# Performance work log

Hardware: AMD Instinct MI355X
Metric: run time of the kernel (lower is better)

## Reference

```python
import jax, jax.numpy as jnp
import numpy as np

B = 131072
D = 256
N_SC = 16
SC_CAP = 2
MAX_USERS = 8
POW_DIM = 10


def setup_inputs() -> dict:
    key = jax.random.key(0)
    k0, k1, k2, k3 = jax.random.split(key, 4)
    x = jax.random.normal(k0, (B, D), dtype=jnp.float32)
    available_actions = jax.random.randint(k1, (B, 2 * MAX_USERS), 0, 2).astype(jnp.int32)
    # per-head Categorical weights: Linear(D, action_dim), small init (gain=0.01 orthogonal-ish)
    W_sc = jax.random.normal(k2, (MAX_USERS, D, N_SC), dtype=jnp.float32) * 0.01
    b_sc = jnp.zeros((MAX_USERS, N_SC), dtype=jnp.float32)
    W_pow = jax.random.normal(k3, (MAX_USERS, D, POW_DIM), dtype=jnp.float32) * 0.01
    b_pow = jnp.zeros((MAX_USERS, POW_DIM), dtype=jnp.float32)
    return {"x": x, "available_actions": available_actions,
            "W_sc": W_sc, "b_sc": b_sc, "W_pow": W_pow, "b_pow": b_pow}


def reference(x, available_actions, W_sc, b_sc, W_pow, b_pow):
    # NOMA branch of MultiDiscreteACTLayer.forward (deterministic=False).
    Bn = x.shape[0]
    key = jax.random.key(42)
    sc_keys = jax.random.split(key, MAX_USERS)
    pow_key = jax.random.fold_in(key, 999)

    NEG = jnp.float32(-1e10)

    def sc_step(sc_stat, inp):
        W, b, avail, k = inp  # W:[D,N_SC], b:[N_SC], avail:[Bn] float, k: key
        logits = x @ W + b                       # [Bn, N_SC]
        mask = sc_stat < SC_CAP                  # subchannel still has capacity
        logits = jnp.where(mask, logits, NEG)
        action = jax.random.categorical(k, logits)        # [Bn] int
        logp = jnp.take_along_axis(jax.nn.log_softmax(logits, -1),
                                   action[:, None], axis=-1)[:, 0]
        # availability masking: unavailable -> action=-1, logp=0
        action = jnp.where(avail > 0, action, -1)
        logp = logp * avail
        # scatter: sc_stat[b, action] += 1 where action != -1
        upd = jnp.where((action >= 0)[:, None],
                        jax.nn.one_hot(jnp.maximum(action, 0), N_SC, dtype=sc_stat.dtype),
                        jnp.zeros((), sc_stat.dtype))
        return sc_stat + upd, (action, logp)

    sc_stat0 = jnp.zeros((Bn, N_SC), dtype=x.dtype)
    avail_f = available_actions.astype(x.dtype)
    avail_sc = avail_f[:, :MAX_USERS].T          # [MAX_USERS, Bn]
    _, (sc_actions, sc_logps) = jax.lax.scan(
        sc_step, sc_stat0, (W_sc, b_sc, avail_sc, sc_keys))

    # power heads: no mask, no loop-carried state -> fully batched
    pow_logits = jnp.einsum('bd,hdk->bhk', x, W_pow) + b_pow   # [Bn, H, POW_DIM]
    pow_actions = jax.random.categorical(pow_key, pow_logits)  # [Bn, H]
    pow_logps = jnp.take_along_axis(jax.nn.log_softmax(pow_logits, -1),
                                    pow_actions[..., None], axis=-1)[..., 0]
    avail_pow = avail_f[:, MAX_USERS:]
    pow_actions = jnp.where(avail_pow > 0, pow_actions, -1)
    pow_logps = pow_logps * avail_pow

    actions = jnp.concatenate([sc_actions.T, pow_actions], axis=-1)          # [Bn, 16]
    action_log_probs = jnp.concatenate([sc_logps.T, pow_logps], axis=-1)
    action_log_probs = jnp.sum(action_log_probs, axis=-1, keepdims=True)     # [Bn, 1]
    return actions, action_log_probs, available_actions
```

## Files before the change

kernel.cpp:

```cpp
#include <hip/hip_runtime.h>


#define B_TOTAL 131072
#define NCOL    208
#define ROWS    32
#define TINYF   1.17549435e-38f

#define WPLANE  53248
#define XB_L    8448
#define XB_P    264

typedef float f32x4 __attribute__((ext_vector_type(4)));
typedef short short8 __attribute__((ext_vector_type(8)));

#define MFMA_BF16(A,B,C) __builtin_amdgcn_mfma_f32_16x16x32_bf16((A),(B),(C),0,0,0)

struct TF2 { unsigned a, b; };

__host__ __device__ constexpr unsigned rotl_(unsigned x, int r) {
  return (x << r) | (x >> (32 - r));
}

__host__ __device__ constexpr TF2 tf2(unsigned k0, unsigned k1, unsigned x0, unsigned x1) {
  unsigned ks0 = k0, ks1 = k1, ks2 = k0 ^ k1 ^ 0x1BD11BDAu;
  x0 += ks0; x1 += ks1;
  x0 += x1; x1 = rotl_(x1, 13); x1 ^= x0;
  x0 += x1; x1 = rotl_(x1, 15); x1 ^= x0;
  x0 += x1; x1 = rotl_(x1, 26); x1 ^= x0;
  x0 += x1; x1 = rotl_(x1,  6); x1 ^= x0;
  x0 += ks1; x1 += ks2 + 1u;
  x0 += x1; x1 = rotl_(x1, 17); x1 ^= x0;
  x0 += x1; x1 = rotl_(x1, 29); x1 ^= x0;
  x0 += x1; x1 = rotl_(x1, 16); x1 ^= x0;
  x0 += x1; x1 = rotl_(x1, 24); x1 ^= x0;
  x0 += ks2; x1 += ks0 + 2u;
  x0 += x1; x1 = rotl_(x1, 13); x1 ^= x0;
  x0 += x1; x1 = rotl_(x1, 15); x1 ^= x0;
  x0 += x1; x1 = rotl_(x1, 26); x1 ^= x0;
  x0 += x1; x1 = rotl_(x1,  6); x1 ^= x0;
  x0 += ks0; x1 += ks1 + 3u;
  x0 += x1; x1 = rotl_(x1, 17); x1 ^= x0;
  x0 += x1; x1 = rotl_(x1, 29); x1 ^= x0;
  x0 += x1; x1 = rotl_(x1, 16); x1 ^= x0;
  x0 += x1; x1 = rotl_(x1, 24); x1 ^= x0;
  x0 += ks1; x1 += ks2 + 4u;
  x0 += x1; x1 = rotl_(x1, 13); x1 ^= x0;
  x0 += x1; x1 = rotl_(x1, 15); x1 ^= x0;
  x0 += x1; x1 = rotl_(x1, 26); x1 ^= x0;
  x0 += x1; x1 = rotl_(x1,  6); x1 ^= x0;
  x0 += ks2; x1 += ks0 + 5u;
  return TF2{x0, x1};
}

__host__ __device__ constexpr unsigned key_a(unsigned d) { return tf2(0u, 42u, 0u, d).a; }
__host__ __device__ constexpr unsigned key_b(unsigned d) { return tf2(0u, 42u, 0u, d).b; }

constexpr unsigned SK0c[8] = {
  key_a(0), key_a(1), key_a(2), key_a(3), key_a(4), key_a(5), key_a(6), key_a(7)
};
constexpr unsigned SK1c[8] = {
  key_b(0), key_b(1), key_b(2), key_b(3), key_b(4), key_b(5), key_b(6), key_b(7)
};
constexpr unsigned PK0 = key_a(999);
constexpr unsigned PK1 = key_b(999);

__device__ __forceinline__ double dlog(double xd) {
  long long b = __double_as_longlong(xd);
  int e = (int)(b >> 52) - 1023;
  double m = __longlong_as_double((b & 0x000FFFFFFFFFFFFFLL) | 0x3FF0000000000000LL);
  if (m > 1.4142135623730951) { m *= 0.5; e += 1; }
  double mp1 = m + 1.0;
  double r = (double)__builtin_amdgcn_rcpf((float)mp1);
  r = fma(fma(-mp1, r, 1.0), r, r);
  double z  = (m - 1.0) * r;
  double z2 = z * z;
  double p = fma(z2, fma(z2, fma(z2, fma(z2, fma(z2,
              1.0/13.0, 1.0/11.0), 1.0/9.0), 1.0/7.0), 1.0/5.0), 1.0/3.0);
  double lm = fma(2.0 * z, z2 * p, 2.0 * z);
  return fma((double)e, 0.6931471805599453, lm);
}

__device__ __forceinline__ float gumbelf(unsigned bits) {
  float u = __uint_as_float((bits >> 9) | 0x3f800000u) - 1.0f;
  u = u + TINYF;
  u = fmaxf(TINYF, u);
  double nl = -dlog((double)u);
  return -(float)dlog(nl);
}

__global__ void repack_kernel(const float* __restrict__ Wsc, const float* __restrict__ bsc,
                              const float* __restrict__ Wpow, const float* __restrict__ bpow,
                              short* __restrict__ Wb, float* __restrict__ bp) {
  int t = blockIdx.x * 256 + threadIdx.x;
  if (t < 53248) {
    int j    = t & 7;
    int lane = (t >> 3) & 63;
    int c    = (t >> 9) & 7;
    int T    = t >> 12;
    int k    = c * 32 + (lane >> 4) * 8 + j;
    int col  = T * 16 + (lane & 15);
    int u = col / 26, n = col % 26;
    float w = (n < 16) ? Wsc[(u * 256 + k) * 16 + n]
                       : Wpow[(u * 256 + k) * 10 + (n - 16)];
    unsigned b0 = __float_as_uint(w) & 0xFFFF0000u;
    float f1 = w - __uint_as_float(b0);
    unsigned b1 = __float_as_uint(f1) & 0xFFFF0000u;
    float f2 = f1 - __uint_as_float(b1);
    unsigned b2 = __float_as_uint(f2) & 0xFFFF0000u;
    int idx = (T * 8 + c) * 512 + lane * 8 + j;
    Wb[idx]              = (short)(b0 >> 16);
    Wb[WPLANE + idx]     = (short)(b1 >> 16);
    Wb[2 * WPLANE + idx] = (short)(b2 >> 16);
  } else {
    int cc = t - 53248;
    float v = 0.f;
    if (cc < NCOL) {
      int u = cc / 26, n = cc % 26;
      v = (n < 16) ? bsc[u * 16 + n] : bpow[u * 10 + (n - 16)];
    }
    bp[cc] = v;
  }
}

__global__ __launch_bounds__(512, 4) void act_kernel(
    const float* __restrict__ x, const int* __restrict__ avail,
    const short* __restrict__ Wb, const float* __restrict__ bp,
    float* __restrict__ out) {
  __shared__ __align__(16) union SMem {
    short xb[3][ROWS][XB_P];
    float gg[ROWS][NCOL];
  } sm;
  __shared__ float lg[ROWS][NCOL];

  const int t = threadIdx.x;
  const int b0 = blockIdx.x * ROWS;

#pragma unroll
  for (int i = 0; i < 4; ++i) {
    int flat = t + 512 * i;
    int r  = flat >> 6;
    int kq = flat & 63;
    float4 v = ((const float4*)(x + (size_t)(b0 + r) * 256))[kq];
    unsigned L0[4], L1[4], L2[4];
#pragma unroll
    for (int e = 0; e < 4; ++e) {
      float f = (&v.x)[e];
      unsigned h0 = __float_as_uint(f) & 0xFFFF0000u;
      float f1 = f - __uint_as_float(h0);
      unsigned h1 = __float_as_uint(f1) & 0xFFFF0000u;
      float f2 = f1 - __uint_as_float(h1);
      unsigned h2 = __float_as_uint(f2) & 0xFFFF0000u;
      L0[e] = h0; L1[e] = h1; L2[e] = h2;
    }
    int ks = 4 * kq;
    *(uint2*)&sm.xb[0][r][ks] =
        make_uint2((L0[0] >> 16) | (L0[1] & 0xFFFF0000u),
                   (L0[2] >> 16) | (L0[3] & 0xFFFF0000u));
    *(uint2*)&sm.xb[1][r][ks] =
        make_uint2((L1[0] >> 16) | (L1[1] & 0xFFFF0000u),
                   (L1[2] >> 16) | (L1[3] & 0xFFFF0000u));
    *(uint2*)&sm.xb[2][r][ks] =
        make_uint2((L2[0] >> 16) | (L2[1] & 0xFFFF0000u),
                   (L2[2] >> 16) | (L2[3] & 0xFFFF0000u));
  }
  __syncthreads();

  {
    const int lane64 = t & 63;
    const int wv  = t >> 6;
    const int w4  = wv & 3;
    const int rh  = wv >> 2;
    const int q   = lane64 >> 4;
    const int r16 = lane64 & 15;
    const int h   = blockIdx.x & 3;
    const bool heavy = (w4 == h);
    const int toff = 3 * w4 + ((w4 > h) ? 1 : 0);

    const f32x4 fz = {0.f, 0.f, 0.f, 0.f};
    f32x4 aM0 = fz, aM1 = fz, aM2 = fz, aM3 = fz;
    f32x4 aS0 = fz, aS1 = fz, aS2 = fz, aS3 = fz;

    const short* xr = &sm.xb[0][rh * 16 + r16][0];
    const int wlane = lane64 * 8;

#pragma unroll 1
    for (int c = 0; c < 8; ++c) {
      const int xo = c * 32 + q * 8;
      short8 x0 = *(const short8*)(xr + xo);
      short8 x1 = *(const short8*)(xr + XB_L + xo);
      short8 x2 = *(const short8*)(xr + 2 * XB_L + xo);
      const int wbase = (toff * 8 + c) * 512 + wlane;

#define DO_TILE(WI, AM, AS) do {                                        \
        short8 w0 = *(const short8*)(Wb + (WI));                        \
        short8 w1 = *(const short8*)(Wb + WPLANE + (WI));               \
        short8 w2 = *(const short8*)(Wb + 2 * WPLANE + (WI));           \
        AM = MFMA_BF16(x0, w0, AM);                                     \
        AS = MFMA_BF16(x1, w0, AS);                                     \
        AS = MFMA_BF16(x0, w1, AS);                                     \
        AS = MFMA_BF16(x1, w1, AS);                                     \
        AS = MFMA_BF16(x2, w0, AS);                                     \
        AS = MFMA_BF16(x0, w2, AS);                                     \
        AS = MFMA_BF16(x2, w1, AS);                                     \
        AS = MFMA_BF16(x1, w2, AS);                                     \
      } while (0)

      DO_TILE(wbase,        aM0, aS0);
      DO_TILE(wbase + 4096, aM1, aS1);
      DO_TILE(wbase + 8192, aM2, aS2);
      if (heavy) DO_TILE(wbase + 12288, aM3, aS3);
#undef DO_TILE
    }

    {
      short8 pa = {0, 0, 0, 0, 0, 0, 0, 0};
      short8 pb = {0, 0, 0, 0, 0, 0, 0, 0};
      if (q == 0) {
        pa[0] = (short)(__float_as_uint((float)r16) >> 16);
        pb[0] = (short)0x3F80;
      }
      f32x4 pr = MFMA_BF16(pa, pb, fz);
      f32x4 pc = MFMA_BF16(pb, pa, fz);
#pragma unroll
      for (int r = 0; r < 4; ++r) {
        int i  = ((int)(pr[r] + 0.5f)) & 15;
        int jo = ((int)(pc[r] + 0.5f)) & 15;
        int gi = rh * 16 + i;
        int c0 = toff * 16 + jo;
        lg[gi][c0     ] = aM0[r] + (aS0[r] + bp[c0]);
        lg[gi][c0 + 16] = aM1[r] + (aS1[r] + bp[c0 + 16]);
        lg[gi][c0 + 32] = aM2[r] + (aS2[r] + bp[c0 + 32]);
        if (heavy)
          lg[gi][c0 + 48] = aM3[r] + (aS3[r] + bp[c0 + 48]);
      }
    }
  }
  __syncthreads();

  {
    const int prow = t >> 4;
    const int pn   = t & 15;
    const unsigned cnt = (unsigned)((b0 + prow) * 16 + pn);
    float* grow = &sm.gg[prow][pn];
#pragma unroll
    for (int u = 0; u < 8; ++u) {
      TF2 r = tf2(SK0c[u], SK1c[u], 0u, cnt);
      grow[u * 26] = gumbelf(r.a ^ r.b);
    }
  }
#pragma unroll
  for (int i = 0; i < 5; ++i) {
    int flat = t + 512 * i;
    int prw  = (flat * 13108) >> 20;
    int q80  = flat - prw * 80;
    int hh   = (q80 * 103) >> 10;
    int jj   = q80 - hh * 10;
    unsigned cnt = (unsigned)((b0 + prw) * 80 + q80);
    TF2 r = tf2(PK0, PK1, 0u, cnt);
    sm.gg[prw][hh * 26 + 16 + jj] = gumbelf(r.a ^ r.b);
  }
  __syncthreads();

  const int row  = t >> 4;
  const int lane = t & 15;
  const int g16  = (t & 63) >> 4;
  const int gb   = b0 + row;
  const int av = avail[gb * 16 + lane];
  int stat = 0;
  float lpsum = 0.0f;
  float my_act = 0.0f;

  for (int u = 0; u < 8; ++u) {
    float logit = lg[row][u * 26 + lane];
    float ml = (stat < 2) ? logit : -1e10f;
    float y  = ml + sm.gg[row][u * 26 + lane];
    float vmax = y;
    for (int off = 8; off; off >>= 1) vmax = fmaxf(vmax, __shfl_xor(vmax, off, 16));
    unsigned long long bal = __ballot(y == vmax);
    int idx = __builtin_ctzll((bal >> (g16 * 16)) & 0xFFFFull);
    float s = __expf(ml);
    for (int off = 8; off; off >>= 1) s += __shfl_xor(s, off, 16);
    float mlidx = __shfl(ml, idx, 16);
    float lp = mlidx - __logf(s);
    int au = __shfl(av, u, 16);
    if (au > 0) {
      lpsum += lp;
      if (lane == idx) stat += 1;
    }
    if (lane == u) my_act = (au > 0) ? (float)idx : -1.0f;
  }

  for (int h = 0; h < 8; ++h) {
    bool on = lane < 10;
    float logit = on ? lg[row][h * 26 + 16 + lane] : -3.0e38f;
    float y     = on ? (logit + sm.gg[row][h * 26 + 16 + lane]) : -3.0e38f;
    float vmax = y;
    for (int off = 8; off; off >>= 1) vmax = fmaxf(vmax, __shfl_xor(vmax, off, 16));
    unsigned long long bal = __ballot(y == vmax);
    int idx = __builtin_ctzll((bal >> (g16 * 16)) & 0xFFFFull);
    float s = on ? __expf(logit) : 0.0f;
    for (int off = 8; off; off >>= 1) s += __shfl_xor(s, off, 16);
    float mlidx = __shfl(logit, idx, 16);
    float lp = mlidx - __logf(s);
    int ah = __shfl(av, 8 + h, 16);
    if (ah > 0) lpsum += lp;
    if (lane == 8 + h) my_act = (ah > 0) ? (float)idx : -1.0f;
  }

  out[(size_t)gb * 16 + lane] = my_act;
  if (lane == 0) out[(size_t)B_TOTAL * 16 + gb] = lpsum;
  out[(size_t)B_TOTAL * 17 + (size_t)gb * 16 + lane] = (float)av;
}

extern "C" void kernel_launch(void* const* d_in, const int* in_sizes, int n_in,
                              void* d_out, int out_size, void* d_ws, size_t ws_size,
                              hipStream_t stream) {
  const float* x    = (const float*)d_in[0];
  const int*   av   = (const int*)  d_in[1];
  const float* Wsc  = (const float*)d_in[2];
  const float* bsc  = (const float*)d_in[3];
  const float* Wpow = (const float*)d_in[4];
  const float* bpow = (const float*)d_in[5];
  float* outp = (float*)d_out;

  float* bp = (float*)d_ws;
  short* Wb = (short*)((char*)d_ws + 1024);

  repack_kernel<<<209, 256, 0, stream>>>(Wsc, bsc, Wpow, bpow, Wb, bp);
  act_kernel<<<B_TOTAL / ROWS, 512, 0, stream>>>(x, av, Wb, bp, outp);
}
```

Measured before the change: 389.7 us.

## Reassign MFMA tiles to cover both row halves and use DPP row reductions

Each wave now owns one or two column tiles across all 32 rows, so every weight fragment loaded from global memory feeds both 16-row halves, halving weight-load traffic per MFMA. The tile ownership is rotated per block to spread the uneven heavy work. The sampling loop swaps shfl_xor reductions for DPP row_ror reductions, takes availability bits from a single ballot, and keeps subchannel Gumbel noise in registers while power noise goes into a smaller shared array. Costs are more accumulator registers and LDS reads of both x halves per wave, which may affect occupancy at the launch bounds.

Result: faster. 375.9 us (-3.5%).

```diff
diff --git a/kernel.cpp b/kernel.cpp
--- a/kernel.cpp
+++ b/kernel.cpp
@@ -14,6 +14,24 @@
 typedef short short8 __attribute__((ext_vector_type(8)));
 
 #define MFMA_BF16(A,B,C) __builtin_amdgcn_mfma_f32_16x16x32_bf16((A),(B),(C),0,0,0)
+
+#define ROR16(v, n) __uint_as_float((unsigned)__builtin_amdgcn_update_dpp(     \
+    (int)__float_as_uint(v), (int)__float_as_uint(v), 0x120 | (n), 0xF, 0xF, false))
+
+__device__ __forceinline__ float redmax16(float v) {
+  v = fmaxf(v, ROR16(v, 8));
+  v = fmaxf(v, ROR16(v, 4));
+  v = fmaxf(v, ROR16(v, 2));
+  v = fmaxf(v, ROR16(v, 1));
+  return v;
+}
+__device__ __forceinline__ float redsum16(float v) {
+  v += ROR16(v, 8);
+  v += ROR16(v, 4);
+  v += ROR16(v, 2);
+  v += ROR16(v, 1);
+  return v;
+}
 
 struct TF2 { unsigned a, b; };
 
@@ -122,13 +140,24 @@
   }
 }
 
+#define PROD8(X0, X1, X2, W0, W1, W2, AM, AS) do {                      \
+    AM = MFMA_BF16(X0, W0, AM);                                         \
+    AS = MFMA_BF16(X1, W0, AS);                                         \
+    AS = MFMA_BF16(X0, W1, AS);                                         \
+    AS = MFMA_BF16(X1, W1, AS);                                         \
+    AS = MFMA_BF16(X2, W0, AS);                                         \
+    AS = MFMA_BF16(X0, W2, AS);                                         \
+    AS = MFMA_BF16(X2, W1, AS);                                         \
+    AS = MFMA_BF16(X1, W2, AS);                                         \
+  } while (0)
+
 __global__ __launch_bounds__(512, 4) void act_kernel(
     const float* __restrict__ x, const int* __restrict__ avail,
     const short* __restrict__ Wb, const float* __restrict__ bp,
     float* __restrict__ out) {
   __shared__ __align__(16) union SMem {
     short xb[3][ROWS][XB_P];
-    float gg[ROWS][NCOL];
+    float gpow[ROWS][80];
   } sm;
   __shared__ float lg[ROWS][NCOL];
 
@@ -168,48 +197,45 @@
   {
     const int lane64 = t & 63;
     const int wv  = t >> 6;
-    const int w4  = wv & 3;
-    const int rh  = wv >> 2;
     const int q   = lane64 >> 4;
     const int r16 = lane64 & 15;
-    const int h   = blockIdx.x & 3;
-    const bool heavy = (w4 == h);
-    const int toff = 3 * w4 + ((w4 > h) ? 1 : 0);
+    const int tA  = (wv + (blockIdx.x & 7)) & 7;
+    const bool heavy = tA < 5;
+    const int tB  = 8 + tA;
 
     const f32x4 fz = {0.f, 0.f, 0.f, 0.f};
-    f32x4 aM0 = fz, aM1 = fz, aM2 = fz, aM3 = fz;
-    f32x4 aS0 = fz, aS1 = fz, aS2 = fz, aS3 = fz;
-
-    const short* xr = &sm.xb[0][rh * 16 + r16][0];
+    f32x4 mA0 = fz, sA0 = fz, mA1 = fz, sA1 = fz;
+    f32x4 mB0 = fz, sB0 = fz, mB1 = fz, sB1 = fz;
+
+    const short* xr0 = &sm.xb[0][r16][0];
+    const short* xr1 = &sm.xb[0][16 + r16][0];
     const int wlane = lane64 * 8;
 
 #pragma unroll 1
     for (int c = 0; c < 8; ++c) {
       const int xo = c * 32 + q * 8;
-      short8 x0 = *(const short8*)(xr + xo);
-      short8 x1 = *(const short8*)(xr + XB_L + xo);
-      short8 x2 = *(const short8*)(xr + 2 * XB_L + xo);
-      const int wbase = (toff * 8 + c) * 512 + wlane;
-
-#define DO_TILE(WI, AM, AS) do {                                        \
-        short8 w0 = *(const short8*)(Wb + (WI));                        \
-        short8 w1 = *(const short8*)(Wb + WPLANE + (WI));               \
-        short8 w2 = *(const short8*)(Wb + 2 * WPLANE + (WI));           \
-        AM = MFMA_BF16(x0, w0, AM);                                     \
-        AS = MFMA_BF16(x1, w0, AS);                                     \
-        AS = MFMA_BF16(x0, w1, AS);                                     \
-        AS = MFMA_BF16(x1, w1, AS);                                     \
-        AS = MFMA_BF16(x2, w0, AS);                                     \
-        AS = MFMA_BF16(x0, w2, AS);                                     \
-        AS = MFMA_BF16(x2, w1, AS);                                     \
-        AS = MFMA_BF16(x1, w2, AS);                                     \
-      } while (0)
-
-      DO_TILE(wbase,        aM0, aS0);
-      DO_TILE(wbase + 4096, aM1, aS1);
-      DO_TILE(wbase + 8192, aM2, aS2);
-      if (heavy) DO_TILE(wbase + 12288, aM3, aS3);
-#undef DO_TILE
+      short8 a0 = *(const short8*)(xr0 + xo);
+      short8 a1 = *(const short8*)(xr0 + XB_L + xo);
+      short8 a2 = *(const short8*)(xr0 + 2 * XB_L + xo);
+      short8 c0_ = *(const short8*)(xr1 + xo);
+      short8 c1_ = *(const short8*)(xr1 + XB_L + xo);
+      short8 c2_ = *(const short8*)(xr1 + 2 * XB_L + xo);
+      {
+        const int wi = (tA * 8 + c) * 512 + wlane;
+        short8 w0 = *(const short8*)(Wb + wi);
+        short8 w1 = *(const short8*)(Wb + WPLANE + wi);
+        short8 w2 = *(const short8*)(Wb + 2 * WPLANE + wi);
+        PROD8(a0,  a1,  a2,  w0, w1, w2, mA0, sA0);
+        PROD8(c0_, c1_, c2_, w0, w1, w2, mA1, sA1);
+      }
+      if (heavy) {
+        const int wi = (tB * 8 + c) * 512 + wlane;
+        short8 w0 = *(const short8*)(Wb + wi);
+        short8 w1 = *(const short8*)(Wb + WPLANE + wi);
+        short8 w2 = *(const short8*)(Wb + 2 * WPLANE + wi);
+        PROD8(a0,  a1,  a2,  w0, w1, w2, mB0, sB0);
+        PROD8(c0_, c1_, c2_, w0, w1, w2, mB1, sB1);
+      }
     }
 
     {
@@ -225,86 +251,86 @@
       for (int r = 0; r < 4; ++r) {
         int i  = ((int)(pr[r] + 0.5f)) & 15;
         int jo = ((int)(pc[r] + 0.5f)) & 15;
-        int gi = rh * 16 + i;
-        int c0 = toff * 16 + jo;
-        lg[gi][c0     ] = aM0[r] + (aS0[r] + bp[c0]);
-        lg[gi][c0 + 16] = aM1[r] + (aS1[r] + bp[c0 + 16]);
-        lg[gi][c0 + 32] = aM2[r] + (aS2[r] + bp[c0 + 32]);
-        if (heavy)
-          lg[gi][c0 + 48] = aM3[r] + (aS3[r] + bp[c0 + 48]);
+        int cA = tA * 16 + jo;
+        lg[i][cA]      = mA0[r] + (sA0[r] + bp[cA]);
+        lg[16 + i][cA] = mA1[r] + (sA1[r] + bp[cA]);
+        if (heavy) {
+          int cB = tB * 16 + jo;
+          lg[i][cB]      = mB0[r] + (sB0[r] + bp[cB]);
+          lg[16 + i][cB] = mB1[r] + (sB1[r] + bp[cB]);
+        }
       }
     }
   }
-  __syncthreads();
-
+
+  float gsc[8];
   {
     const int prow = t >> 4;
     const int pn   = t & 15;
     const unsigned cnt = (unsigned)((b0 + prow) * 16 + pn);
-    float* grow = &sm.gg[prow][pn];
 #pragma unroll
     for (int u = 0; u < 8; ++u) {
       TF2 r = tf2(SK0c[u], SK1c[u], 0u, cnt);
-      grow[u * 26] = gumbelf(r.a ^ r.b);
-    }
-  }
+      gsc[u] = gumbelf(r.a ^ r.b);
+    }
+  }
+  __syncthreads();
+
 #pragma unroll
   for (int i = 0; i < 5; ++i) {
     int flat = t + 512 * i;
     int prw  = (flat * 13108) >> 20;
     int q80  = flat - prw * 80;
-    int hh   = (q80 * 103) >> 10;
-    int jj   = q80 - hh * 10;
     unsigned cnt = (unsigned)((b0 + prw) * 80 + q80);
     TF2 r = tf2(PK0, PK1, 0u, cnt);
-    sm.gg[prw][hh * 26 + 16 + jj] = gumbelf(r.a ^ r.b);
+    sm.gpow[prw][q80] = gumbelf(r.a ^ r.b);
   }
   __syncthreads();
 
   const int row  = t >> 4;
   const int lane = t & 15;
   const int g16  = (t & 63) >> 4;
+  const int shamt = g16 * 16;
   const int gb   = b0 + row;
   const int av = avail[gb * 16 + lane];
+  const unsigned avm = (unsigned)((__ballot(av > 0) >> shamt) & 0xFFFFull);
   int stat = 0;
   float lpsum = 0.0f;
   float my_act = 0.0f;
 
+#pragma unroll
   for (int u = 0; u < 8; ++u) {
     float logit = lg[row][u * 26 + lane];
     float ml = (stat < 2) ? logit : -1e10f;
-    float y  = ml + sm.gg[row][u * 26 + lane];
-    float vmax = y;
-    for (int off = 8; off; off >>= 1) vmax = fmaxf(vmax, __shfl_xor(vmax, off, 16));
+    float y  = ml + gsc[u];
+    float vmax = redmax16(y);
     unsigned long long bal = __ballot(y == vmax);
-    int idx = __builtin_ctzll((bal >> (g16 * 16)) & 0xFFFFull);
-    float s = __expf(ml);
-    for (int off = 8; off; off >>= 1) s += __shfl_xor(s, off, 16);
-    float mlidx = __shfl(ml, idx, 16);
+    int idx = __builtin_ctz((unsigned)((bal >> shamt) & 0xFFFFull));
+    float s = redsum16(__expf(ml));
+    float mlidx = redmax16((lane == idx) ? ml : -3.0e38f);
     float lp = mlidx - __logf(s);
-    int au = __shfl(av, u, 16);
-    if (au > 0) {
+    int au = (int)((avm >> u) & 1u);
+    if (au) {
       lpsum += lp;
       if (lane == idx) stat += 1;
     }
-    if (lane == u) my_act = (au > 0) ? (float)idx : -1.0f;
-  }
-
+    if (lane == u) my_act = au ? (float)idx : -1.0f;
+  }
+
+#pragma unroll
   for (int h = 0; h < 8; ++h) {
     bool on = lane < 10;
     float logit = on ? lg[row][h * 26 + 16 + lane] : -3.0e38f;
-    float y     = on ? (logit + sm.gg[row][h * 26 + 16 + lane]) : -3.0e38f;
-    float vmax = y;
-    for (int off = 8; off; off >>= 1) vmax = fmaxf(vmax, __shfl_xor(vmax, off, 16));
+    float y     = on ? (logit + sm.gpow[row][h * 10 + lane]) : -3.0e38f;
+    float vmax = redmax16(y);
     unsigned long long bal = __ballot(y == vmax);
-    int idx = __builtin_ctzll((bal >> (g16 * 16)) & 0xFFFFull);
-    float s = on ? __expf(logit) : 0.0f;
-    for (int off = 8; off; off >>= 1) s += __shfl_xor(s, off, 16);
-    float mlidx = __shfl(logit, idx, 16);
+    int idx = __builtin_ctz((unsigned)((bal >> shamt) & 0xFFFFull));
+    float s = redsum16(on ? __expf(logit) : 0.0f);
+    float mlidx = redmax16((lane == idx) ? logit : -3.0e38f);
     float lp = mlidx - __logf(s);
-    int ah = __shfl(av, 8 + h, 16);
-    if (ah > 0) lpsum += lp;
-    if (lane == 8 + h) my_act = (ah > 0) ? (float)idx : -1.0f;
+    int ah = (int)((avm >> (8 + h)) & 1u);
+    if (ah) lpsum += lp;
+    if (lane == 8 + h) my_act = ah ? (float)idx : -1.0f;
   }
 
   out[(size_t)gb * 16 + lane] = my_act;
```
